# Kernel tuning notes

Measured on AMD Instinct MI355X. Metric: run time of the kernel, lower is better.

## Reference

```python
import jax, jax.numpy as jnp
import numpy as np

NEG_SLOPE = 0.2


def gat_conv(x, src, dst, W, att_src, att_dst, bias, heads, out_ch, concat):
    # PyG GATConv (add_self_loops handled by caller). x: [N, in], W: [heads*out, in]
    N = x.shape[0]
    xw = (x @ W.T).reshape(N, heads, out_ch)                  # [N, H, C]
    a_src = jnp.sum(xw * att_src, axis=-1)                    # [N, H]
    a_dst = jnp.sum(xw * att_dst, axis=-1)                    # [N, H]
    alpha = a_src[src] + a_dst[dst]                           # [E, H]
    alpha = jax.nn.leaky_relu(alpha, NEG_SLOPE)
    # segment softmax over incoming edges of each dst node
    amax = jax.ops.segment_max(alpha, dst, num_segments=N)    # [N, H]
    amax = jnp.where(jnp.isfinite(amax), amax, 0.0)
    e = jnp.exp(alpha - amax[dst])                            # [E, H]
    denom = jax.ops.segment_sum(e, dst, num_segments=N)       # [N, H]
    coef = e / (denom[dst] + 1e-16)                           # [E, H]
    msg = xw[src] * coef[..., None]                           # [E, H, C]
    out = jax.ops.segment_sum(msg, dst, num_segments=N)       # [N, H, C]
    if concat:
        out = out.reshape(N, heads * out_ch)
    else:
        out = out.mean(axis=1)
    return out + bias


def setup_inputs() -> dict:
    key = jax.random.key(0)
    ks = jax.random.split(key, 10)
    N, E, F_IN, H, C = 50000, 1600000, 128, 4, 32
    x = jax.random.normal(ks[0], (N, F_IN), dtype=jnp.float32)
    edge_index = jax.random.randint(ks[1], (2, E), 0, N, dtype=jnp.int64)
    s1 = 1.0 / np.sqrt(F_IN)
    W1 = jax.random.uniform(ks[2], (H * C, F_IN), jnp.float32, -s1, s1)
    att_src1 = jax.random.normal(ks[3], (1, H, C), jnp.float32) * 0.1
    att_dst1 = jax.random.normal(ks[4], (1, H, C), jnp.float32) * 0.1
    b1 = jnp.zeros((H * C,), jnp.float32)
    s2 = 1.0 / np.sqrt(H * C)
    W2 = jax.random.uniform(ks[5], (1, H * C), jnp.float32, -s2, s2)
    att_src2 = jax.random.normal(ks[6], (1, 1, 1), jnp.float32) * 0.1
    att_dst2 = jax.random.normal(ks[7], (1, 1, 1), jnp.float32) * 0.1
    b2 = jnp.zeros((1,), jnp.float32)
    return {"x": x, "edge_index": edge_index, "W1": W1, "att_src1": att_src1,
            "att_dst1": att_dst1, "b1": b1, "W2": W2, "att_src2": att_src2,
            "att_dst2": att_dst2, "b2": b2}


def reference(x, edge_index, W1, att_src1, att_dst1, b1, W2, att_src2, att_dst2, b2):
    N = x.shape[0]
    loops = jnp.arange(N, dtype=edge_index.dtype)
    src = jnp.concatenate([edge_index[0], loops])
    dst = jnp.concatenate([edge_index[1], loops])
    h = gat_conv(x, src, dst, W1, att_src1, att_dst1, b1, heads=4, out_ch=32, concat=True)
    h = jax.nn.relu(h)
    out = gat_conv(h, src, dst, W2, att_src2, att_dst2, b2, heads=1, out_ch=1, concat=False)
    return out.squeeze(-1)
```

## Files before the change

kernel.cpp:

```cpp
#include <hip/hip_runtime.h>
#include <hip/hip_bf16.h>
#include <hip/hip_fp16.h>
#include <cstdint>
#include <cstddef>
#include <math.h>

#define NEG_SLOPE 0.2f
#define SLOTS 96
#define BSHIFT 7
#define BCAP 5632
#define SCB 288
#define ECHUNK 5760

typedef __attribute__((ext_vector_type(8))) _Float16 f16x8;
typedef __attribute__((ext_vector_type(4))) float f32x4;

__device__ __forceinline__ float lrelu(float x) { return x > 0.f ? x : NEG_SLOPE * x; }


__global__ __launch_bounds__(256) void k_init(const float* __restrict__ W1,
                                              __half* __restrict__ W1h,
                                              int* __restrict__ bin_cnt, int nbin)
{
    int i = blockIdx.x * 256 + threadIdx.x;
    if (i < 128 * 128) W1h[i] = (__half)W1[i];
    if (i < nbin) bin_cnt[i] = 0;
}

__global__ __launch_bounds__(256) void k_gemm_scatter(
    const float* __restrict__ x, const __half* __restrict__ W1h,
    const float* __restrict__ att_src, const float* __restrict__ att_dst,
    const int* __restrict__ ei, int E, int N, int GB,
    __half* __restrict__ xw, float* __restrict__ a_src, float* __restrict__ a_dst,
    int* __restrict__ bin_cnt, unsigned* __restrict__ binned)
{
    __shared__ union {
        struct { __half tile[64][136]; float s_as[128]; float s_ad[128]; } g;
        unsigned sc[ECHUNK + 3 * 400];
    } sm;

    if (blockIdx.x >= GB) {
        const int Et = E + N;
        const int nbin = (N + 127) >> BSHIFT;
        unsigned* ledge = sm.sc;
        int* lhist = (int*)(ledge + ECHUNK);
        int* lbase = lhist + nbin;
        int* lpos  = lbase + nbin;
        const int bi = blockIdx.x - GB;
        const int chunk = (Et + SCB - 1) / SCB;
        const int e0 = bi * chunk;
        const int e1 = (e0 + chunk) < Et ? (e0 + chunk) : Et;
        for (int i = threadIdx.x; i < nbin; i += 256) { lhist[i] = 0; lpos[i] = 0; }
        __syncthreads();
        for (int e = e0 + threadIdx.x; e < e1; e += 256) {
            int s, d;
            if (e < E) { s = ei[e]; d = ei[(size_t)E + e]; }
            else       { s = d = e - E; }
            unsigned b = (unsigned)d >> BSHIFT;
            ledge[e - e0] = (b << 23) | ((unsigned)(d & 127) << 16) | (unsigned)s;
            atomicAdd(&lhist[b], 1);
        }
        __syncthreads();
        for (int i = threadIdx.x; i < nbin; i += 256)
            lbase[i] = lhist[i] ? atomicAdd(&bin_cnt[i], lhist[i]) : 0;
        __syncthreads();
        const int ne = e1 - e0;
        for (int i = threadIdx.x; i < ne; i += 256) {
            unsigned w = ledge[i];
            unsigned b = w >> 23;
            int p = lbase[b] + atomicAdd(&lpos[b], 1);
            if (p < BCAP)
                binned[(size_t)b * BCAP + p] = w & 0x7FFFFFu;
        }
        return;
    }

    const int tid = threadIdx.x;
    if (tid < 128) { sm.g.s_as[tid] = att_src[tid]; sm.g.s_ad[tid] = att_dst[tid]; }

    const int wv = tid >> 6, lane = tid & 63;
    const int rl = lane & 15, g = lane >> 4;
    const int bm = blockIdx.x * 64;
    const int row = bm + wv * 16 + rl;
    const int rr = row < N ? row : N - 1;
    const float* xr = x + (size_t)rr * 128 + g * 8;

    f32x4 acc[8];
    #pragma unroll
    for (int i = 0; i < 8; i++) acc[i] = (f32x4){0.f, 0.f, 0.f, 0.f};

    #pragma unroll
    for (int k0 = 0; k0 < 128; k0 += 32) {
        float4 fa0 = *(const float4*)(xr + k0);
        float4 fa1 = *(const float4*)(xr + k0 + 4);
        f16x8 a;
        a[0] = (_Float16)fa0.x; a[1] = (_Float16)fa0.y;
        a[2] = (_Float16)fa0.z; a[3] = (_Float16)fa0.w;
        a[4] = (_Float16)fa1.x; a[5] = (_Float16)fa1.y;
        a[6] = (_Float16)fa1.z; a[7] = (_Float16)fa1.w;
        #pragma unroll
        for (int ct = 0; ct < 8; ct++) {
            f16x8 b = *(const f16x8*)(W1h + (size_t)(ct * 16 + rl) * 128 + k0 + g * 8);
            acc[ct] = __builtin_amdgcn_mfma_f32_16x16x32_f16(a, b, acc[ct], 0, 0, 0);
        }
    }
    #pragma unroll
    for (int ct = 0; ct < 8; ct++)
        #pragma unroll
        for (int r = 0; r < 4; r++)
            sm.g.tile[wv * 16 + g * 4 + r][ct * 16 + rl] = (__half)acc[ct][r];
    __syncthreads();

    {
        int r = tid >> 2, h = tid & 3;
        int n = bm + r;
        if (n < N) {
            float4 vv[4];
            vv[0] = *(const float4*)&sm.g.tile[r][h * 32];
            vv[1] = *(const float4*)&sm.g.tile[r][h * 32 + 8];
            vv[2] = *(const float4*)&sm.g.tile[r][h * 32 + 16];
            vv[3] = *(const float4*)&sm.g.tile[r][h * 32 + 24];
            __half* xo = xw + (size_t)n * 128 + h * 32;
            *(float4*)(xo)      = vv[0];
            *(float4*)(xo + 8)  = vv[1];
            *(float4*)(xo + 16) = vv[2];
            *(float4*)(xo + 24) = vv[3];
            const float4* asp = (const float4*)(sm.g.s_as + h * 32);
            const float4* adp = (const float4*)(sm.g.s_ad + h * 32);
            float sv = 0.f, dv = 0.f;
            #pragma unroll
            for (int q = 0; q < 4; q++) {
                const __half2* hp = (const __half2*)&vv[q];
                float2 f0 = __half22float2(hp[0]);
                float2 f1 = __half22float2(hp[1]);
                float2 f2 = __half22float2(hp[2]);
                float2 f3 = __half22float2(hp[3]);
                float4 A0 = asp[2 * q], A1 = asp[2 * q + 1];
                float4 D0 = adp[2 * q], D1 = adp[2 * q + 1];
                sv += f0.x * A0.x + f0.y * A0.y + f1.x * A0.z + f1.y * A0.w
                    + f2.x * A1.x + f2.y * A1.y + f3.x * A1.z + f3.y * A1.w;
                dv += f0.x * D0.x + f0.y * D0.y + f1.x * D0.z + f1.y * D0.w
                    + f2.x * D1.x + f2.y * D1.y + f3.x * D1.z + f3.y * D1.w;
            }
            a_src[n * 4 + h] = sv;
            a_dst[n * 4 + h] = dv;
        }
    }
}

__global__ __launch_bounds__(512) void k_bin2bucket(
    const unsigned* __restrict__ binned, const int* __restrict__ bin_cnt,
    int* __restrict__ cnt, unsigned short* __restrict__ bucket, int N)
{
    __shared__ int lcnt[128];
    __shared__ unsigned short lb[128][SLOTS];
    const int tid = threadIdx.x;
    const int b = blockIdx.x;
    const int base_d = b << BSHIFT;
    if (tid < 128) lcnt[tid] = 0;
    __syncthreads();
    int bc = bin_cnt[b]; bc = bc < BCAP ? bc : BCAP;
    const unsigned* src = binned + (size_t)b * BCAP;
    for (int t = tid; t < bc; t += 512) {
        unsigned w = src[t];
        int dl = (int)(w >> 16);
        int p = atomicAdd(&lcnt[dl], 1);
        if (p < SLOTS) lb[dl][p] = (unsigned short)(w & 0xFFFFu);
    }
    __syncthreads();
    {
        int dl = tid >> 2, j = tid & 3;
        int d = base_d + dl;
        if (dl < 128 && d < N) {
            int deg = lcnt[dl]; deg = deg < SLOTS ? deg : SLOTS;
            if (j == 0) cnt[d] = deg;
            unsigned* go = (unsigned*)(bucket + (size_t)d * SLOTS);
            const unsigned* lrow = (const unsigned*)lb[dl];
            int nw = (deg + 1) >> 1;
            for (int i = j; i < nw; i += 4) go[i] = lrow[i];
        }
    }
}

__global__ __launch_bounds__(256) void k_agg(const __half* __restrict__ xw,
                                             const float* __restrict__ a_src,
                                             const float* __restrict__ a_dst,
                                             const int* __restrict__ cnt,
                                             const unsigned short* __restrict__ bucket,
                                             const float* __restrict__ b1,
                                             const float* __restrict__ W2,
                                             float* __restrict__ xw2, int N)
{
    const int wv = threadIdx.x >> 6, lane = threadIdx.x & 63;
    const int es = lane >> 4, cl = lane & 15;
    const int d = blockIdx.x * 4 + wv;
    if (d >= N) return;
    const int head = cl >> 2;
    int deg = cnt[d]; deg = deg < SLOTS ? deg : SLOTS;
    const unsigned short* brow = bucket + (size_t)d * SLOTS;

    float4 ad4 = ((const float4*)a_dst)[d];
    float adh = (head & 2) ? ((head & 1) ? ad4.w : ad4.z)
                           : ((head & 1) ? ad4.y : ad4.x);

    float acc[8] = {};
    float csum = 0.f;
    const int jb = 4 * es;
    for (int k = 0; k < deg; k += 16) {
        ushort4 ss = *(const ushort4*)(brow + k + jb);
        bool v0 = (k + jb + 0) < deg, v1 = (k + jb + 1) < deg;
        bool v2 = (k + jb + 2) < deg, v3 = (k + jb + 3) < deg;
        int s0 = v0 ? (int)ss.x : 0;
        int s1 = v1 ? (int)ss.y : 0;
        int s2 = v2 ? (int)ss.z : 0;
        int s3 = v3 ? (int)ss.w : 0;
        float ash0 = a_src[4 * s0 + head];
        float ash1 = a_src[4 * s1 + head];
        float ash2 = a_src[4 * s2 + head];
        float ash3 = a_src[4 * s3 + head];
        float4 x0 = *(const float4*)(xw + (size_t)s0 * 128 + cl * 8);
        float4 x1 = *(const float4*)(xw + (size_t)s1 * 128 + cl * 8);
        float4 x2 = *(const float4*)(xw + (size_t)s2 * 128 + cl * 8);
        float4 x3 = *(const float4*)(xw + (size_t)s3 * 128 + cl * 8);
        float c0 = v0 ? __expf(lrelu(ash0 + adh)) : 0.f;
        float c1 = v1 ? __expf(lrelu(ash1 + adh)) : 0.f;
        float c2 = v2 ? __expf(lrelu(ash2 + adh)) : 0.f;
        float c3 = v3 ? __expf(lrelu(ash3 + adh)) : 0.f;
        const __half2* h0 = (const __half2*)&x0;
        const __half2* h1 = (const __half2*)&x1;
        const __half2* h2 = (const __half2*)&x2;
        const __half2* h3 = (const __half2*)&x3;
        #pragma unroll
        for (int q = 0; q < 4; q++) {
            float2 f0 = __half22float2(h0[q]);
            float2 f1 = __half22float2(h1[q]);
            float2 f2 = __half22float2(h2[q]);
            float2 f3 = __half22float2(h3[q]);
            acc[2*q]   = fmaf(c0, f0.x, acc[2*q]);
            acc[2*q+1] = fmaf(c0, f0.y, acc[2*q+1]);
            acc[2*q]   = fmaf(c1, f1.x, acc[2*q]);
            acc[2*q+1] = fmaf(c1, f1.y, acc[2*q+1]);
            acc[2*q]   = fmaf(c2, f2.x, acc[2*q]);
            acc[2*q+1] = fmaf(c2, f2.y, acc[2*q+1]);
            acc[2*q]   = fmaf(c3, f3.x, acc[2*q]);
            acc[2*q+1] = fmaf(c3, f3.y, acc[2*q+1]);
        }
        csum += (c0 + c1) + (c2 + c3);
    }
    #pragma unroll
    for (int q = 0; q < 8; q++) {
        acc[q] += __shfl_xor(acc[q], 16);
        acc[q] += __shfl_xor(acc[q], 32);
    }
    csum += __shfl_xor(csum, 16);
    csum += __shfl_xor(csum, 32);

    float inv = 1.f / (csum + 1e-16f);
    float4 bb0 = ((const float4*)b1)[cl * 2], bb1 = ((const float4*)b1)[cl * 2 + 1];
    float4 ww0 = ((const float4*)W2)[cl * 2], ww1 = ((const float4*)W2)[cl * 2 + 1];
    float t = fmaxf(fmaf(acc[0], inv, bb0.x), 0.f) * ww0.x
            + fmaxf(fmaf(acc[1], inv, bb0.y), 0.f) * ww0.y
            + fmaxf(fmaf(acc[2], inv, bb0.z), 0.f) * ww0.z
            + fmaxf(fmaf(acc[3], inv, bb0.w), 0.f) * ww0.w
            + fmaxf(fmaf(acc[4], inv, bb1.x), 0.f) * ww1.x
            + fmaxf(fmaf(acc[5], inv, bb1.y), 0.f) * ww1.y
            + fmaxf(fmaf(acc[6], inv, bb1.z), 0.f) * ww1.z
            + fmaxf(fmaf(acc[7], inv, bb1.w), 0.f) * ww1.w;
    #pragma unroll
    for (int off = 1; off < 16; off <<= 1) t += __shfl_xor(t, off);
    if (lane == 0) xw2[d] = t;
}

__global__ __launch_bounds__(256) void k_layer2(const float* __restrict__ xw2,
                                                const int* __restrict__ cnt,
                                                const unsigned short* __restrict__ bucket,
                                                const float* __restrict__ att_src2,
                                                const float* __restrict__ att_dst2,
                                                const float* __restrict__ b2,
                                                float* __restrict__ out, int N)
{
    int grpi = (blockIdx.x * blockDim.x + threadIdx.x) >> 6;
    int lane = threadIdx.x & 63;
    int sub  = lane >> 4, li = lane & 15;
    int d    = grpi * 4 + sub;
    if (d >= N) return;
    float as2  = att_src2[0];
    float adst = xw2[d] * att_dst2[0];
    int deg = cnt[d]; deg = deg < SLOTS ? deg : SLOTS;
    const unsigned short* brow = bucket + (size_t)d * SLOTS;
    float l = 0.f, acc = 0.f;
    for (int j = 4 * li; j < deg; j += 64) {
        ushort4 ss = *(const ushort4*)(brow + j);
        int s0 = (int)ss.x;
        bool v1 = (j + 1) < deg, v2 = (j + 2) < deg, v3 = (j + 3) < deg;
        int s1 = v1 ? (int)ss.y : 0;
        int s2 = v2 ? (int)ss.z : 0;
        int s3 = v3 ? (int)ss.w : 0;
        float xs0 = xw2[s0];
        float xs1 = xw2[s1];
        float xs2 = xw2[s2];
        float xs3 = xw2[s3];
        float p0 = __expf(lrelu(fmaf(xs0, as2, adst)));
        float p1 = v1 ? __expf(lrelu(fmaf(xs1, as2, adst))) : 0.f;
        float p2 = v2 ? __expf(lrelu(fmaf(xs2, as2, adst))) : 0.f;
        float p3 = v3 ? __expf(lrelu(fmaf(xs3, as2, adst))) : 0.f;
        l += (p0 + p1) + (p2 + p3);
        acc = fmaf(p0, xs0, fmaf(p1, xs1, fmaf(p2, xs2, fmaf(p3, xs3, acc))));
    }
    #pragma unroll
    for (int off = 1; off < 16; off <<= 1) {
        l   += __shfl_xor(l, off);
        acc += __shfl_xor(acc, off);
    }
    if (li == 0) out[d] = acc / (l + 1e-16f) + b2[0];
}

extern "C" void kernel_launch(void* const* d_in, const int* in_sizes, int n_in,
                              void* d_out, int out_size, void* d_ws, size_t ws_size,
                              hipStream_t stream)
{
    const float* x        = (const float*)d_in[0];
    const int*   ei       = (const int*)d_in[1];
    const float* W1       = (const float*)d_in[2];
    const float* att_src1 = (const float*)d_in[3];
    const float* att_dst1 = (const float*)d_in[4];
    const float* b1       = (const float*)d_in[5];
    const float* W2       = (const float*)d_in[6];
    const float* att_src2 = (const float*)d_in[7];
    const float* att_dst2 = (const float*)d_in[8];
    const float* b2       = (const float*)d_in[9];
    float* out = (float*)d_out;

    const int N  = in_sizes[0] / 128;
    const int E  = in_sizes[1] / 2;
    const int NBIN = (N + 127) >> BSHIFT;

    char* p = (char*)d_ws;
    auto alloc = [&](size_t bytes) {
        char* r = p;
        p += (bytes + 255) & ~(size_t)255;
        return (void*)r;
    };
    __half* xw    = (__half*)alloc((size_t)N * 128 * 2);
    __half* W1h   = (__half*)alloc((size_t)128 * 128 * 2);
    float* a_src  = (float*)alloc((size_t)N * 4 * 4);
    float* a_dst  = (float*)alloc((size_t)N * 4 * 4);
    float* xw2    = (float*)alloc((size_t)N * 4);
    int*   cnt    = (int*)alloc((size_t)N * 4);
    unsigned short* bucket = (unsigned short*)alloc((size_t)N * SLOTS * 2);
    unsigned* binned = (unsigned*)alloc((size_t)NBIN * BCAP * 4);
    int* bin_cnt  = (int*)alloc((size_t)NBIN * 4);

    const int GB = (N + 63) / 64;
    k_init        <<<64,          256, 0, stream>>>(W1, W1h, bin_cnt, NBIN);
    k_gemm_scatter<<<GB + SCB,    256, 0, stream>>>(x, W1h, att_src1, att_dst1, ei,
                                                    E, N, GB, xw, a_src, a_dst,
                                                    bin_cnt, binned);
    k_bin2bucket  <<<NBIN,        512, 0, stream>>>(binned, bin_cnt, cnt, bucket, N);
    k_agg         <<<(N + 3)/4,   256, 0, stream>>>(xw, a_src, a_dst, cnt, bucket,
                                                    b1, W2, xw2, N);
    k_layer2      <<<(N + 15)/16, 256, 0, stream>>>(xw2, cnt, bucket, att_src2,
                                                    att_dst2, b2, out, N);
}
```

Before: 187.1 us.

## Fuse all stages into one cooperative persistent kernel with grid syncs

Replaces the five separate kernel launches with a single cooperative persistent kernel that runs init, GEMM+edge binning, bin-to-bucket, layer-1 aggregation and layer-2 aggregation as phases separated by grid.sync. This removes per-launch overhead and inter-kernel gaps. The grid is limited to resident blocks (up to 8 per CU), so each phase loops over its work items, and it pays for grid-wide barriers. It also retunes the scatter block count and chunk size, and falls back to the old multi-kernel path if the cooperative launch fails.

```diff
diff --git a/kernel.cpp b/kernel.cpp
--- a/kernel.cpp
+++ b/kernel.cpp
@@ -1,22 +1,312 @@
 #include <hip/hip_runtime.h>
 #include <hip/hip_bf16.h>
 #include <hip/hip_fp16.h>
+#include <hip/hip_cooperative_groups.h>
 #include <cstdint>
 #include <cstddef>
 #include <math.h>
+
+namespace cg = cooperative_groups;
 
 #define NEG_SLOPE 0.2f
 #define SLOTS 96
 #define BSHIFT 7
 #define BCAP 5632
-#define SCB 288
-#define ECHUNK 5760
+#define SCB 304
+#define ECHUNK 5440
+#define NCU 256
 
 typedef __attribute__((ext_vector_type(8))) _Float16 f16x8;
 typedef __attribute__((ext_vector_type(4))) float f32x4;
 
 __device__ __forceinline__ float lrelu(float x) { return x > 0.f ? x : NEG_SLOPE * x; }
 
+
+__global__ __launch_bounds__(256, 4) void k_fused(
+    const float* __restrict__ x, const int* __restrict__ ei,
+    const float* __restrict__ W1,
+    const float* __restrict__ att_src1, const float* __restrict__ att_dst1,
+    const float* __restrict__ b1, const float* __restrict__ W2,
+    const float* __restrict__ att_src2, const float* __restrict__ att_dst2,
+    const float* __restrict__ b2, float* __restrict__ out,
+    __half* __restrict__ xw, __half* __restrict__ W1h,
+    float* __restrict__ a_src, float* __restrict__ a_dst,
+    float* __restrict__ xw2, int* __restrict__ cnt,
+    unsigned short* __restrict__ bucket, unsigned* __restrict__ binned,
+    int* __restrict__ bin_cnt, int E, int N, int GB, int nbin)
+{
+    cg::grid_group grid = cg::this_grid();
+    __shared__ union SM {
+        struct { __half tile[64][136]; float s_as[128]; float s_ad[128]; } g;
+        struct { unsigned ledge[ECHUNK]; int lhist[400]; int lbase[400]; int lpos[400]; } s;
+        struct { int lcnt[128]; unsigned short lb[128][SLOTS]; } b;
+    } sm;
+
+    const int tid = threadIdx.x;
+    const int bid = blockIdx.x;
+    const int G = gridDim.x;
+
+    for (int i = bid * 256 + tid; i < 128 * 128; i += G * 256) W1h[i] = (__half)W1[i];
+    for (int i = bid * 256 + tid; i < nbin; i += G * 256) bin_cnt[i] = 0;
+    __threadfence();
+    grid.sync();
+
+    for (int job = bid; job < GB + SCB; job += G) {
+        if (job < GB) {
+            if (tid < 128) { sm.g.s_as[tid] = att_src1[tid]; sm.g.s_ad[tid] = att_dst1[tid]; }
+            const int wv = tid >> 6, lane = tid & 63;
+            const int rl = lane & 15, g = lane >> 4;
+            const int bm = job * 64;
+            const int row = bm + wv * 16 + rl;
+            const int rr = row < N ? row : N - 1;
+            const float* xr = x + (size_t)rr * 128 + g * 8;
+
+            f32x4 acc[8];
+            #pragma unroll
+            for (int i = 0; i < 8; i++) acc[i] = (f32x4){0.f, 0.f, 0.f, 0.f};
+
+            #pragma unroll
+            for (int k0 = 0; k0 < 128; k0 += 32) {
+                float4 fa0 = *(const float4*)(xr + k0);
+                float4 fa1 = *(const float4*)(xr + k0 + 4);
+                f16x8 a;
+                a[0] = (_Float16)fa0.x; a[1] = (_Float16)fa0.y;
+                a[2] = (_Float16)fa0.z; a[3] = (_Float16)fa0.w;
+                a[4] = (_Float16)fa1.x; a[5] = (_Float16)fa1.y;
+                a[6] = (_Float16)fa1.z; a[7] = (_Float16)fa1.w;
+                #pragma unroll
+                for (int ct = 0; ct < 8; ct++) {
+                    f16x8 b = *(const f16x8*)(W1h + (size_t)(ct * 16 + rl) * 128 + k0 + g * 8);
+                    acc[ct] = __builtin_amdgcn_mfma_f32_16x16x32_f16(a, b, acc[ct], 0, 0, 0);
+                }
+            }
+            #pragma unroll
+            for (int ct = 0; ct < 8; ct++)
+                #pragma unroll
+                for (int r = 0; r < 4; r++)
+                    sm.g.tile[wv * 16 + g * 4 + r][ct * 16 + rl] = (__half)acc[ct][r];
+            __syncthreads();
+
+            int r = tid >> 2, h = tid & 3;
+            int n = bm + r;
+            if (n < N) {
+                float4 vv[4];
+                vv[0] = *(const float4*)&sm.g.tile[r][h * 32];
+                vv[1] = *(const float4*)&sm.g.tile[r][h * 32 + 8];
+                vv[2] = *(const float4*)&sm.g.tile[r][h * 32 + 16];
+                vv[3] = *(const float4*)&sm.g.tile[r][h * 32 + 24];
+                __half* xo = xw + (size_t)n * 128 + h * 32;
+                *(float4*)(xo)      = vv[0];
+                *(float4*)(xo + 8)  = vv[1];
+                *(float4*)(xo + 16) = vv[2];
+                *(float4*)(xo + 24) = vv[3];
+                const float4* asp = (const float4*)(sm.g.s_as + h * 32);
+                const float4* adp = (const float4*)(sm.g.s_ad + h * 32);
+                float sv = 0.f, dv = 0.f;
+                #pragma unroll
+                for (int q = 0; q < 4; q++) {
+                    const __half2* hp = (const __half2*)&vv[q];
+                    float2 f0 = __half22float2(hp[0]);
+                    float2 f1 = __half22float2(hp[1]);
+                    float2 f2 = __half22float2(hp[2]);
+                    float2 f3 = __half22float2(hp[3]);
+                    float4 A0 = asp[2 * q], A1 = asp[2 * q + 1];
+                    float4 D0 = adp[2 * q], D1 = adp[2 * q + 1];
+                    sv += f0.x * A0.x + f0.y * A0.y + f1.x * A0.z + f1.y * A0.w
+                        + f2.x * A1.x + f2.y * A1.y + f3.x * A1.z + f3.y * A1.w;
+                    dv += f0.x * D0.x + f0.y * D0.y + f1.x * D0.z + f1.y * D0.w
+                        + f2.x * D1.x + f2.y * D1.y + f3.x * D1.z + f3.y * D1.w;
+                }
+                a_src[n * 4 + h] = sv;
+                a_dst[n * 4 + h] = dv;
+            }
+        } else {
+            const int Et = E + N;
+            const int bi = job - GB;
+            const int chunk = (Et + SCB - 1) / SCB;
+            const int e0 = bi * chunk;
+            const int e1 = (e0 + chunk) < Et ? (e0 + chunk) : Et;
+            for (int i = tid; i < nbin; i += 256) { sm.s.lhist[i] = 0; sm.s.lpos[i] = 0; }
+            __syncthreads();
+            for (int e = e0 + tid; e < e1; e += 256) {
+                int s, d;
+                if (e < E) { s = ei[e]; d = ei[(size_t)E + e]; }
+                else       { s = d = e - E; }
+                unsigned b = (unsigned)d >> BSHIFT;
+                sm.s.ledge[e - e0] = (b << 23) | ((unsigned)(d & 127) << 16) | (unsigned)s;
+                atomicAdd(&sm.s.lhist[b], 1);
+            }
+            __syncthreads();
+            for (int i = tid; i < nbin; i += 256)
+                sm.s.lbase[i] = sm.s.lhist[i] ? atomicAdd(&bin_cnt[i], sm.s.lhist[i]) : 0;
+            __syncthreads();
+            const int ne = e1 - e0;
+            for (int i = tid; i < ne; i += 256) {
+                unsigned w = sm.s.ledge[i];
+                unsigned b = w >> 23;
+                int p = sm.s.lbase[b] + atomicAdd(&sm.s.lpos[b], 1);
+                if (p < BCAP)
+                    binned[(size_t)b * BCAP + p] = w & 0x7FFFFFu;
+            }
+        }
+        __syncthreads();
+    }
+    __threadfence();
+    grid.sync();
+
+    for (int b = bid; b < nbin; b += G) {
+        const int base_d = b << BSHIFT;
+        if (tid < 128) sm.b.lcnt[tid] = 0;
+        __syncthreads();
+        int bc = bin_cnt[b]; bc = bc < BCAP ? bc : BCAP;
+        const unsigned* src = binned + (size_t)b * BCAP;
+        for (int t = tid; t < bc; t += 256) {
+            unsigned w = src[t];
+            int dl = (int)(w >> 16);
+            int p = atomicAdd(&sm.b.lcnt[dl], 1);
+            if (p < SLOTS) sm.b.lb[dl][p] = (unsigned short)(w & 0xFFFFu);
+        }
+        __syncthreads();
+        int dl = tid >> 1, j = tid & 1;
+        int d = base_d + dl;
+        if (dl < 128 && d < N) {
+            int deg = sm.b.lcnt[dl]; deg = deg < SLOTS ? deg : SLOTS;
+            if (j == 0) cnt[d] = deg;
+            unsigned* go = (unsigned*)(bucket + (size_t)d * SLOTS);
+            const unsigned* lrow = (const unsigned*)sm.b.lb[dl];
+            int nw = (deg + 1) >> 1;
+            for (int i = j; i < nw; i += 2) go[i] = lrow[i];
+        }
+        __syncthreads();
+    }
+    __threadfence();
+    grid.sync();
+
+    {
+        const int wv = tid >> 6, lane = tid & 63;
+        const int es = lane >> 4, cl = lane & 15;
+        const int head = cl >> 2;
+        const int jb = 4 * es;
+        const int ngroups = (N + 3) / 4;
+        for (int g = bid; g < ngroups; g += G) {
+            const int d = g * 4 + wv;
+            if (d >= N) continue;
+            int deg = cnt[d]; deg = deg < SLOTS ? deg : SLOTS;
+            const unsigned short* brow = bucket + (size_t)d * SLOTS;
+
+            float4 ad4 = ((const float4*)a_dst)[d];
+            float adh = (head & 2) ? ((head & 1) ? ad4.w : ad4.z)
+                                   : ((head & 1) ? ad4.y : ad4.x);
+            float acc[8] = {};
+            float csum = 0.f;
+            for (int k = 0; k < deg; k += 16) {
+                ushort4 ss = *(const ushort4*)(brow + k + jb);
+                bool v0 = (k + jb + 0) < deg, v1 = (k + jb + 1) < deg;
+                bool v2 = (k + jb + 2) < deg, v3 = (k + jb + 3) < deg;
+                int s0 = v0 ? (int)ss.x : 0;
+                int s1 = v1 ? (int)ss.y : 0;
+                int s2 = v2 ? (int)ss.z : 0;
+                int s3 = v3 ? (int)ss.w : 0;
+                float ash0 = a_src[4 * s0 + head];
+                float ash1 = a_src[4 * s1 + head];
+                float ash2 = a_src[4 * s2 + head];
+                float ash3 = a_src[4 * s3 + head];
+                float4 x0 = *(const float4*)(xw + (size_t)s0 * 128 + cl * 8);
+                float4 x1 = *(const float4*)(xw + (size_t)s1 * 128 + cl * 8);
+                float4 x2 = *(const float4*)(xw + (size_t)s2 * 128 + cl * 8);
+                float4 x3 = *(const float4*)(xw + (size_t)s3 * 128 + cl * 8);
+                float c0 = v0 ? __expf(lrelu(ash0 + adh)) : 0.f;
+                float c1 = v1 ? __expf(lrelu(ash1 + adh)) : 0.f;
+                float c2 = v2 ? __expf(lrelu(ash2 + adh)) : 0.f;
+                float c3 = v3 ? __expf(lrelu(ash3 + adh)) : 0.f;
+                const __half2* h0 = (const __half2*)&x0;
+                const __half2* h1 = (const __half2*)&x1;
+                const __half2* h2 = (const __half2*)&x2;
+                const __half2* h3 = (const __half2*)&x3;
+                #pragma unroll
+                for (int q = 0; q < 4; q++) {
+                    float2 f0 = __half22float2(h0[q]);
+                    float2 f1 = __half22float2(h1[q]);
+                    float2 f2 = __half22float2(h2[q]);
+                    float2 f3 = __half22float2(h3[q]);
+                    acc[2*q]   = fmaf(c0, f0.x, acc[2*q]);
+                    acc[2*q+1] = fmaf(c0, f0.y, acc[2*q+1]);
+                    acc[2*q]   = fmaf(c1, f1.x, acc[2*q]);
+                    acc[2*q+1] = fmaf(c1, f1.y, acc[2*q+1]);
+                    acc[2*q]   = fmaf(c2, f2.x, acc[2*q]);
+                    acc[2*q+1] = fmaf(c2, f2.y, acc[2*q+1]);
+                    acc[2*q]   = fmaf(c3, f3.x, acc[2*q]);
+                    acc[2*q+1] = fmaf(c3, f3.y, acc[2*q+1]);
+                }
+                csum += (c0 + c1) + (c2 + c3);
+            }
+            #pragma unroll
+            for (int q = 0; q < 8; q++) {
+                acc[q] += __shfl_xor(acc[q], 16);
+                acc[q] += __shfl_xor(acc[q], 32);
+            }
+            csum += __shfl_xor(csum, 16);
+            csum += __shfl_xor(csum, 32);
+
+            float inv = 1.f / (csum + 1e-16f);
+            float4 bb0 = ((const float4*)b1)[cl * 2], bb1 = ((const float4*)b1)[cl * 2 + 1];
+            float4 ww0 = ((const float4*)W2)[cl * 2], ww1 = ((const float4*)W2)[cl * 2 + 1];
+            float t = fmaxf(fmaf(acc[0], inv, bb0.x), 0.f) * ww0.x
+                    + fmaxf(fmaf(acc[1], inv, bb0.y), 0.f) * ww0.y
+                    + fmaxf(fmaf(acc[2], inv, bb0.z), 0.f) * ww0.z
+                    + fmaxf(fmaf(acc[3], inv, bb0.w), 0.f) * ww0.w
+                    + fmaxf(fmaf(acc[4], inv, bb1.x), 0.f) * ww1.x
+                    + fmaxf(fmaf(acc[5], inv, bb1.y), 0.f) * ww1.y
+                    + fmaxf(fmaf(acc[6], inv, bb1.z), 0.f) * ww1.z
+                    + fmaxf(fmaf(acc[7], inv, bb1.w), 0.f) * ww1.w;
+            #pragma unroll
+            for (int off = 1; off < 16; off <<= 1) t += __shfl_xor(t, off);
+            if (lane == 0) xw2[d] = t;
+        }
+    }
+    __threadfence();
+    grid.sync();
+
+    {
+        const int wv = tid >> 6, lane = tid & 63;
+        const int sub = lane >> 4, li = lane & 15;
+        const float as2  = att_src2[0];
+        const float ad2  = att_dst2[0];
+        const int nw4 = (N + 3) / 4;
+        for (int w = bid * 4 + wv; w < nw4; w += G * 4) {
+            int d = w * 4 + sub;
+            if (d >= N) continue;
+            float adst = xw2[d] * ad2;
+            int deg = cnt[d]; deg = deg < SLOTS ? deg : SLOTS;
+            const unsigned short* brow = bucket + (size_t)d * SLOTS;
+            float l = 0.f, acc = 0.f;
+            for (int j = 4 * li; j < deg; j += 64) {
+                ushort4 ss = *(const ushort4*)(brow + j);
+                int s0 = (int)ss.x;
+                bool v1 = (j + 1) < deg, v2 = (j + 2) < deg, v3 = (j + 3) < deg;
+                int s1 = v1 ? (int)ss.y : 0;
+                int s2 = v2 ? (int)ss.z : 0;
+                int s3 = v3 ? (int)ss.w : 0;
+                float xs0 = xw2[s0];
+                float xs1 = xw2[s1];
+                float xs2 = xw2[s2];
+                float xs3 = xw2[s3];
+                float p0 = __expf(lrelu(fmaf(xs0, as2, adst)));
+                float p1 = v1 ? __expf(lrelu(fmaf(xs1, as2, adst))) : 0.f;
+                float p2 = v2 ? __expf(lrelu(fmaf(xs2, as2, adst))) : 0.f;
+                float p3 = v3 ? __expf(lrelu(fmaf(xs3, as2, adst))) : 0.f;
+                l += (p0 + p1) + (p2 + p3);
+                acc = fmaf(p0, xs0, fmaf(p1, xs1, fmaf(p2, xs2, fmaf(p3, xs3, acc))));
+            }
+            #pragma unroll
+            for (int off = 1; off < 16; off <<= 1) {
+                l   += __shfl_xor(l, off);
+                acc += __shfl_xor(acc, off);
+            }
+            if (li == 0) out[d] = acc / (l + 1e-16f) + b2[0];
+        }
+    }
+}
 
 __global__ __launch_bounds__(256) void k_init(const float* __restrict__ W1,
                                               __half* __restrict__ W1h,
@@ -36,39 +326,35 @@
 {
     __shared__ union {
         struct { __half tile[64][136]; float s_as[128]; float s_ad[128]; } g;
-        unsigned sc[ECHUNK + 3 * 400];
+        struct { unsigned ledge[ECHUNK]; int lhist[400]; int lbase[400]; int lpos[400]; } s;
     } sm;
 
     if (blockIdx.x >= GB) {
         const int Et = E + N;
         const int nbin = (N + 127) >> BSHIFT;
-        unsigned* ledge = sm.sc;
-        int* lhist = (int*)(ledge + ECHUNK);
-        int* lbase = lhist + nbin;
-        int* lpos  = lbase + nbin;
         const int bi = blockIdx.x - GB;
         const int chunk = (Et + SCB - 1) / SCB;
         const int e0 = bi * chunk;
         const int e1 = (e0 + chunk) < Et ? (e0 + chunk) : Et;
-        for (int i = threadIdx.x; i < nbin; i += 256) { lhist[i] = 0; lpos[i] = 0; }
+        for (int i = threadIdx.x; i < nbin; i += 256) { sm.s.lhist[i] = 0; sm.s.lpos[i] = 0; }
         __syncthreads();
         for (int e = e0 + threadIdx.x; e < e1; e += 256) {
             int s, d;
             if (e < E) { s = ei[e]; d = ei[(size_t)E + e]; }
             else       { s = d = e - E; }
             unsigned b = (unsigned)d >> BSHIFT;
-            ledge[e - e0] = (b << 23) | ((unsigned)(d & 127) << 16) | (unsigned)s;
-            atomicAdd(&lhist[b], 1);
+            sm.s.ledge[e - e0] = (b << 23) | ((unsigned)(d & 127) << 16) | (unsigned)s;
+            atomicAdd(&sm.s.lhist[b], 1);
         }
         __syncthreads();
         for (int i = threadIdx.x; i < nbin; i += 256)
-            lbase[i] = lhist[i] ? atomicAdd(&bin_cnt[i], lhist[i]) : 0;
+            sm.s.lbase[i] = sm.s.lhist[i] ? atomicAdd(&bin_cnt[i], sm.s.lhist[i]) : 0;
         __syncthreads();
         const int ne = e1 - e0;
         for (int i = threadIdx.x; i < ne; i += 256) {
-            unsigned w = ledge[i];
+            unsigned w = sm.s.ledge[i];
             unsigned b = w >> 23;
-            int p = lbase[b] + atomicAdd(&lpos[b], 1);
+            int p = sm.s.lbase[b] + atomicAdd(&sm.s.lpos[b], 1);
             if (p < BCAP)
                 binned[(size_t)b * BCAP + p] = w & 0x7FFFFFu;
         }
@@ -77,7 +363,6 @@
 
     const int tid = threadIdx.x;
     if (tid < 128) { sm.g.s_as[tid] = att_src[tid]; sm.g.s_ad[tid] = att_dst[tid]; }
-
     const int wv = tid >> 6, lane = tid & 63;
     const int rl = lane & 15, g = lane >> 4;
     const int bm = blockIdx.x * 64;
@@ -88,7 +373,6 @@
     f32x4 acc[8];
     #pragma unroll
     for (int i = 0; i < 8; i++) acc[i] = (f32x4){0.f, 0.f, 0.f, 0.f};
-
     #pragma unroll
     for (int k0 = 0; k0 < 128; k0 += 32) {
         float4 fa0 = *(const float4*)(xr + k0);
@@ -110,7 +394,6 @@
         for (int r = 0; r < 4; r++)
             sm.g.tile[wv * 16 + g * 4 + r][ct * 16 + rl] = (__half)acc[ct][r];
     __syncthreads();
-
     {
         int r = tid >> 2, h = tid & 3;
         int n = bm + r;
@@ -202,7 +485,6 @@
     float4 ad4 = ((const float4*)a_dst)[d];
     float adh = (head & 2) ? ((head & 1) ? ad4.w : ad4.z)
                            : ((head & 1) ? ad4.y : ad4.x);
-
     float acc[8] = {};
     float csum = 0.f;
     const int jb = 4 * es;
@@ -331,9 +613,10 @@
     const float* b2       = (const float*)d_in[9];
     float* out = (float*)d_out;
 
-    const int N  = in_sizes[0] / 128;
-    const int E  = in_sizes[1] / 2;
-    const int NBIN = (N + 127) >> BSHIFT;
+    int N  = in_sizes[0] / 128;
+    int E  = in_sizes[1] / 2;
+    int NBIN = (N + 127) >> BSHIFT;
+    int GB = (N + 63) / 64;
 
     char* p = (char*)d_ws;
     auto alloc = [&](size_t bytes) {
@@ -351,7 +634,29 @@
     unsigned* binned = (unsigned*)alloc((size_t)NBIN * BCAP * 4);
     int* bin_cnt  = (int*)alloc((size_t)NBIN * 4);
 
-    const int GB = (N + 63) / 64;
+    static int coop_grid = 0;
+    if (coop_grid == 0) {
+        int bpc = 0;
+        hipError_t e = hipOccupancyMaxActiveBlocksPerMultiprocessor(
+            &bpc, (const void*)k_fused, 256, 0);
+        if (e != hipSuccess || bpc < 1) coop_grid = -1;
+        else {
+            if (bpc > 8) bpc = 8;
+            coop_grid = bpc * NCU;
+        }
+    }
+
+    if (coop_grid > 0) {
+        void* args[] = { &x, &ei, &W1, &att_src1, &att_dst1, &b1, &W2, &att_src2,
+                         &att_dst2, &b2, &out, &xw, &W1h, &a_src, &a_dst, &xw2,
+                         &cnt, &bucket, &binned, &bin_cnt, &E, &N, &GB, &NBIN };
+        hipError_t e = hipLaunchCooperativeKernel((const void*)k_fused,
+                                                  dim3(coop_grid), dim3(256),
+                                                  args, 0, stream);
+        if (e == hipSuccess) return;
+        coop_grid = -1;
+    }
+
     k_init        <<<64,          256, 0, stream>>>(W1, W1h, bin_cnt, NBIN);
     k_gemm_scatter<<<GB + SCB,    256, 0, stream>>>(x, W1h, att_src1, att_dst1, ei,
                                                     E, N, GB, xw, a_src, a_dst,
```

After: 668.3 us. +257.2%, slower.
